# Optimization experiments

Measured on AMD Instinct MI355X. Metric: run time of the kernel, lower is better.

The kernel has to match this reference:

```python
import jax, jax.numpy as jnp
import numpy as np

N_ORDERS = 4  # edge groups processed sequentially by EmulsionConv


def setup_inputs() -> dict:
    key = jax.random.key(0)
    ks = jax.random.split(key, 12)
    N, E, D_IN, H, D_OUT, ED = 50000, 800000, 10, 64, 10, 1
    s = 0.1
    return {
        "x": jax.random.normal(ks[0], (N, D_IN), jnp.float32),
        "edge_index": jax.random.randint(ks[1], (2, E), 0, N, jnp.int32),
        "edge_features": jax.random.normal(ks[2], (E, ED), jnp.float32),
        "lin0_w": jax.random.normal(ks[3], (D_IN, H), jnp.float32) * s,
        "lin0_b": jnp.zeros((H,), jnp.float32),
        "lin1_w": jax.random.normal(ks[4], (H, H), jnp.float32) * s,
        "lin1_b": jnp.zeros((H,), jnp.float32),
        "lin2_w": jax.random.normal(ks[5], (H, H), jnp.float32) * s,
        "lin2_b": jnp.zeros((H,), jnp.float32),
        "em_w": jax.random.normal(ks[6], (3, 2 * H + ED, H), jnp.float32) * s,
        "em_b": jnp.zeros((3, H), jnp.float32),
        "ec_w": jax.random.normal(ks[7], (3, 2 * H, H), jnp.float32) * s,
        "ec_b": jnp.zeros((3, H), jnp.float32),
        "out_w": jax.random.normal(ks[8], (H, D_OUT), jnp.float32) * s,
        "out_b": jnp.zeros((D_OUT,), jnp.float32),
    }


def _emulsion_conv(x, edge_index, edge_features, w, b):
    # Sequential per-order gather -> MLP message -> scatter-add; direction=0 (aggregate at source).
    N = x.shape[0]
    E = edge_index.shape[1]
    per = E // N_ORDERS
    for i in range(N_ORDERS):
        sl = slice(i * per, (i + 1) * per)
        src = edge_index[0, sl]
        dst = edge_index[1, sl]
        x_j = x[src]  # [per, H]
        x_i = x[dst]  # [per, H]
        msg = jnp.concatenate([x_i, x_j - x_i, edge_features[sl]], axis=1)
        msg = jax.nn.relu(msg @ w + b)
        agg = jax.ops.segment_sum(msg, src, num_segments=N)
        x = (x + agg) / 2.0
    return x


def _edge_conv(x, edge_index, w, b):
    # EdgeConv: nn([x_i, x_j - x_i]) with max aggregation at target nodes.
    N = x.shape[0]
    src, dst = edge_index[0], edge_index[1]
    x_i = x[dst]
    x_j = x[src]
    msg = jax.nn.relu(jnp.concatenate([x_i, x_j - x_i], axis=1) @ w + b)
    agg = jax.ops.segment_max(msg, dst, num_segments=N)
    return jnp.where(jnp.isfinite(agg), agg, 0.0)  # empty segments -> 0


def reference(x, edge_index, edge_features,
              lin0_w, lin0_b, lin1_w, lin1_b, lin2_w, lin2_b,
              em_w, em_b, ec_w, ec_b, out_w, out_b):
    lin_ws = [lin0_w, lin1_w, lin2_w]
    lin_bs = [lin0_b, lin1_b, lin2_b]
    for i in range(3):
        x = jax.nn.relu(x @ lin_ws[i] + lin_bs[i])
        x = _emulsion_conv(x, edge_index, edge_features, em_w[i], em_b[i])
    for i in range(3):
        x = _edge_conv(x, edge_index, ec_w[i], ec_b[i])
    return x @ out_w + out_b
```

## Files before the change

### kernel.cpp

```cpp
#include <hip/hip_runtime.h>
#include <hip/hip_fp16.h>


#define NN 50000
#define NE 800000
#define PER 200000
#define HD 64
#define NKEY 250112
#define GB_CNT 3125
#define GB_PREP 192
#define GB_LIN 782
#define GB_KEYS 977

typedef _Float16 half8 __attribute__((ext_vector_type(8)));
typedef float float4v __attribute__((ext_vector_type(4)));

struct UvLds {
    _Float16 wuh[64 * 72], wul[64 * 72], wvh[64 * 72], wvl[64 * 72];
    _Float16 rp[4 * 16 * 72];
};

__global__ __launch_bounds__(256) void k_front(
        const int* __restrict__ ei, int* __restrict__ cnt,
        uchar2* __restrict__ rank,
        const float* __restrict__ em_w, const float* __restrict__ ec_w,
        _Float16* __restrict__ wh,
        const float* __restrict__ xin, const float* __restrict__ W0,
        const float* __restrict__ b0, float* __restrict__ x) {
    __shared__ float xs[64][11];
    int t = threadIdx.x;
    if (blockIdx.x < GB_CNT) {
        int e = blockIdx.x * 256 + t;
        int src = ei[e];
        int dst = ei[NE + e];
        int o = e / PER;
        int r1 = atomicAdd(&cnt[o * NN + src], 1);
        int r2 = atomicAdd(&cnt[4 * NN + dst], 1);
        rank[e] = make_uchar2((unsigned char)r1, (unsigned char)r2);
    } else if (blockIdx.x < GB_CNT + GB_PREP) {
        int idx = (blockIdx.x - GB_CNT) * 256 + t;
        int mat = idx >> 12, pos = idx & 4095;
        int n = pos >> 6, k = pos & 63;
        float val;
        if (mat < 3)      { const float* B = em_w + mat * 129 * 64;     val = B[k*64+n] - B[(64+k)*64+n]; }
        else if (mat < 6) { const float* B = em_w + (mat-3) * 129 * 64; val = B[(64+k)*64+n]; }
        else if (mat < 9) { const float* B = ec_w + (mat-6) * 128 * 64; val = B[k*64+n] - B[(64+k)*64+n]; }
        else              { const float* B = ec_w + (mat-9) * 128 * 64; val = B[(64+k)*64+n]; }
        _Float16 h = (_Float16)val;
        _Float16 l = (_Float16)(val - (float)h);
        wh[(size_t)mat * 4096 + n * 64 + k] = h;
        wh[(size_t)(12 + mat) * 4096 + n * 64 + k] = l;
    } else {
        const int K = 10;
        int n0 = (blockIdx.x - GB_CNT - GB_PREP) * 64;
        for (int idx = t; idx < 64 * K; idx += 256) {
            int n = idx / K, k = idx - n * K;
            int g = n0 + n;
            xs[n][k] = (g < NN) ? xin[(size_t)g * K + k] : 0.f;
        }
        __syncthreads();
        int ng = t >> 4;
        int f0 = (t & 15) * 4;
        float acc[4][4] = {};
        for (int k = 0; k < K; ++k) {
            float4 w4 = *(const float4*)&W0[k * HD + f0];
            #pragma unroll
            for (int j = 0; j < 4; ++j) {
                float xv = xs[ng * 4 + j][k];
                acc[j][0] += xv * w4.x; acc[j][1] += xv * w4.y;
                acc[j][2] += xv * w4.z; acc[j][3] += xv * w4.w;
            }
        }
        float4 b4 = *(const float4*)&b0[f0];
        #pragma unroll
        for (int j = 0; j < 4; ++j) {
            int g = n0 + ng * 4 + j;
            if (g < NN) {
                float4 o;
                o.x = fmaxf(acc[j][0] + b4.x, 0.f);
                o.y = fmaxf(acc[j][1] + b4.y, 0.f);
                o.z = fmaxf(acc[j][2] + b4.z, 0.f);
                o.w = fmaxf(acc[j][3] + b4.w, 0.f);
                *(float4*)&x[(size_t)g * HD + f0] = o;
            }
        }
    }
}

__global__ __launch_bounds__(256) void scan_blk(
        const int* __restrict__ cnt, int* __restrict__ bsum) {
    __shared__ int s[256];
    int t = threadIdx.x;
    int i = blockIdx.x * 256 + t;
    int c = (i < NKEY) ? cnt[i] : 0;
    s[t] = c; __syncthreads();
    for (int d = 1; d < 256; d <<= 1) {
        int v = (t >= d) ? s[t - d] : 0;
        __syncthreads(); s[t] += v; __syncthreads();
    }
    if (t == 255) bsum[blockIdx.x] = s[255];
}

__global__ __launch_bounds__(256) void scan_fin2(
        const int* __restrict__ cnt, const int* __restrict__ bsum,
        int* __restrict__ ofs) {
    __shared__ int s[256];
    int t = threadIdx.x;
    int i = blockIdx.x * 256 + t;
    int pre = 0;
    for (int j = t; j < blockIdx.x; j += 256) pre += bsum[j];
    s[t] = pre; __syncthreads();
    for (int d = 128; d > 0; d >>= 1) {
        if (t < d) s[t] += s[t + d];
        __syncthreads();
    }
    int base = s[0];
    __syncthreads();
    int c = (i < NKEY) ? cnt[i] : 0;
    s[t] = c; __syncthreads();
    for (int d = 1; d < 256; d <<= 1) {
        int v = (t >= d) ? s[t - d] : 0;
        __syncthreads(); s[t] += v; __syncthreads();
    }
    if (i < NKEY) ofs[i] = base + s[t] - c;
}

__device__ __forceinline__ void uv_body(
        UvLds& L, int bid, const float* __restrict__ x,
        const _Float16* __restrict__ Wuh, const _Float16* __restrict__ Wul,
        const _Float16* __restrict__ Wvh, const _Float16* __restrict__ Wvl,
        const float* __restrict__ bias,
        _Float16* __restrict__ u, _Float16* __restrict__ v) {
    int t = threadIdx.x;
    int n0 = bid * 64;
    {
        int n = t >> 2, c = (t & 3) * 16;
        *(half8*)&L.wuh[n * 72 + c]     = *(const half8*)&Wuh[n * 64 + c];
        *(half8*)&L.wuh[n * 72 + c + 8] = *(const half8*)&Wuh[n * 64 + c + 8];
        *(half8*)&L.wul[n * 72 + c]     = *(const half8*)&Wul[n * 64 + c];
        *(half8*)&L.wul[n * 72 + c + 8] = *(const half8*)&Wul[n * 64 + c + 8];
        *(half8*)&L.wvh[n * 72 + c]     = *(const half8*)&Wvh[n * 64 + c];
        *(half8*)&L.wvh[n * 72 + c + 8] = *(const half8*)&Wvh[n * 64 + c + 8];
        *(half8*)&L.wvl[n * 72 + c]     = *(const half8*)&Wvl[n * 64 + c];
        *(half8*)&L.wvl[n * 72 + c + 8] = *(const half8*)&Wvl[n * 64 + c + 8];
    }
    int w = t >> 6, lane = t & 63;
    int quad = lane >> 4, l16 = lane & 15;
    int m0 = w * 16;
    int row = n0 + m0 + l16;
    half8 ah0, ah1, al0, al1;
    {
        float f[16];
        if (row < NN) {
            const float4* p = (const float4*)&x[(size_t)row * HD + quad * 8];
            *(float4*)&f[0] = p[0]; *(float4*)&f[4] = p[1];
            const float4* q = (const float4*)&x[(size_t)row * HD + 32 + quad * 8];
            *(float4*)&f[8] = q[0]; *(float4*)&f[12] = q[1];
        } else {
            #pragma unroll
            for (int j = 0; j < 16; ++j) f[j] = 0.f;
        }
        #pragma unroll
        for (int j = 0; j < 8; ++j) {
            _Float16 h = (_Float16)f[j];
            ah0[j] = h; al0[j] = (_Float16)(f[j] - (float)h);
            _Float16 h2 = (_Float16)f[j + 8];
            ah1[j] = h2; al1[j] = (_Float16)(f[j + 8] - (float)h2);
        }
    }
    __syncthreads();

    float4v au[4], av[4];
    #pragma unroll
    for (int nt = 0; nt < 4; ++nt) {
        int n = nt * 16 + l16;
        half8 bh0 = *(half8*)&L.wuh[n * 72 + quad * 8];
        half8 bh1 = *(half8*)&L.wuh[n * 72 + 32 + quad * 8];
        half8 bl0 = *(half8*)&L.wul[n * 72 + quad * 8];
        half8 bl1 = *(half8*)&L.wul[n * 72 + 32 + quad * 8];
        float4v acc = {0.f, 0.f, 0.f, 0.f};
        acc = __builtin_amdgcn_mfma_f32_16x16x32_f16(ah0, bh0, acc, 0, 0, 0);
        acc = __builtin_amdgcn_mfma_f32_16x16x32_f16(ah1, bh1, acc, 0, 0, 0);
        acc = __builtin_amdgcn_mfma_f32_16x16x32_f16(al0, bh0, acc, 0, 0, 0);
        acc = __builtin_amdgcn_mfma_f32_16x16x32_f16(al1, bh1, acc, 0, 0, 0);
        acc = __builtin_amdgcn_mfma_f32_16x16x32_f16(ah0, bl0, acc, 0, 0, 0);
        acc = __builtin_amdgcn_mfma_f32_16x16x32_f16(ah1, bl1, acc, 0, 0, 0);
        au[nt] = acc;
        half8 ch0 = *(half8*)&L.wvh[n * 72 + quad * 8];
        half8 ch1 = *(half8*)&L.wvh[n * 72 + 32 + quad * 8];
        half8 cl0 = *(half8*)&L.wvl[n * 72 + quad * 8];
        half8 cl1 = *(half8*)&L.wvl[n * 72 + 32 + quad * 8];
        float4v accv = {0.f, 0.f, 0.f, 0.f};
        accv = __builtin_amdgcn_mfma_f32_16x16x32_f16(ah0, ch0, accv, 0, 0, 0);
        accv = __builtin_amdgcn_mfma_f32_16x16x32_f16(ah1, ch1, accv, 0, 0, 0);
        accv = __builtin_amdgcn_mfma_f32_16x16x32_f16(al0, ch0, accv, 0, 0, 0);
        accv = __builtin_amdgcn_mfma_f32_16x16x32_f16(al1, ch1, accv, 0, 0, 0);
        accv = __builtin_amdgcn_mfma_f32_16x16x32_f16(ah0, cl0, accv, 0, 0, 0);
        accv = __builtin_amdgcn_mfma_f32_16x16x32_f16(ah1, cl1, accv, 0, 0, 0);
        av[nt] = accv;
    }

    _Float16* rpw = &L.rp[w * 16 * 72];
    #pragma unroll
    for (int nt = 0; nt < 4; ++nt) {
        float bn = bias[nt * 16 + l16];
        #pragma unroll
        for (int r = 0; r < 4; ++r)
            rpw[(quad * 4 + r) * 72 + nt * 16 + l16] = (_Float16)(au[nt][r] + bn);
    }
    int mr = lane >> 2, cr = (lane & 3) * 16;
    int gr = n0 + m0 + mr;
    if (gr < NN) {
        *(half8*)&u[(size_t)gr * HD + cr]     = *(half8*)&rpw[mr * 72 + cr];
        *(half8*)&u[(size_t)gr * HD + cr + 8] = *(half8*)&rpw[mr * 72 + cr + 8];
    }
    #pragma unroll
    for (int nt = 0; nt < 4; ++nt) {
        #pragma unroll
        for (int r = 0; r < 4; ++r)
            rpw[(quad * 4 + r) * 72 + nt * 16 + l16] = (_Float16)(av[nt][r]);
    }
    if (gr < NN) {
        *(half8*)&v[(size_t)gr * HD + cr]     = *(half8*)&rpw[mr * 72 + cr];
        *(half8*)&v[(size_t)gr * HD + cr + 8] = *(half8*)&rpw[mr * 72 + cr + 8];
    }
}

__global__ __launch_bounds__(256) void uv_slim(
        const float* __restrict__ x,
        const _Float16* __restrict__ Wuh, const _Float16* __restrict__ Wul,
        const _Float16* __restrict__ Wvh, const _Float16* __restrict__ Wvl,
        const float* __restrict__ bias,
        _Float16* __restrict__ u, _Float16* __restrict__ v) {
    __shared__ UvLds L;
    uv_body(L, blockIdx.x, x, Wuh, Wul, Wvh, Wvl, bias, u, v);
}

__global__ __launch_bounds__(256) void k_fill_uv(
        const int* __restrict__ ei, const float* __restrict__ ef,
        const int* __restrict__ ofs, const uchar2* __restrict__ rank,
        unsigned* __restrict__ em_val, int* __restrict__ ec_val,
        const float* __restrict__ x,
        const _Float16* __restrict__ Wuh, const _Float16* __restrict__ Wul,
        const _Float16* __restrict__ Wvh, const _Float16* __restrict__ Wvl,
        const float* __restrict__ bias,
        _Float16* __restrict__ u, _Float16* __restrict__ v) {
    __shared__ UvLds L;
    if (blockIdx.x < GB_CNT) {
        int e = blockIdx.x * 256 + threadIdx.x;
        int src = ei[e];
        int dst = ei[NE + e];
        int o = e / PER;
        uchar2 r = rank[e];
        int p1 = ofs[o * NN + src] + r.x;
        unsigned short eb = __half_as_ushort(__float2half_rn(ef[e]));
        em_val[p1] = ((unsigned)dst << 16) | (unsigned)eb;
        int p2 = ofs[4 * NN + dst] + r.y - NE;
        ec_val[p2] = src;
    } else {
        uv_body(L, blockIdx.x - GB_CNT, x, Wuh, Wul, Wvh, Wvl, bias, u, v);
    }
}

__device__ __forceinline__ void load_h8(const __half* p, float* o) {
    float4 r = *(const float4*)p;
    __half2 h0 = *reinterpret_cast<__half2*>(&r.x);
    __half2 h1 = *reinterpret_cast<__half2*>(&r.y);
    __half2 h2 = *reinterpret_cast<__half2*>(&r.z);
    __half2 h3 = *reinterpret_cast<__half2*>(&r.w);
    float2 f0 = __half22float2(h0), f1 = __half22float2(h1);
    float2 f2 = __half22float2(h2), f3 = __half22float2(h3);
    o[0] = f0.x; o[1] = f0.y; o[2] = f1.x; o[3] = f1.y;
    o[4] = f2.x; o[5] = f2.y; o[6] = f3.x; o[7] = f3.y;
}

__device__ __forceinline__ void cvt_h8(float4 r, float* o) {
    __half2 h0 = *reinterpret_cast<__half2*>(&r.x);
    __half2 h1 = *reinterpret_cast<__half2*>(&r.y);
    __half2 h2 = *reinterpret_cast<__half2*>(&r.z);
    __half2 h3 = *reinterpret_cast<__half2*>(&r.w);
    float2 f0 = __half22float2(h0), f1 = __half22float2(h1);
    float2 f2 = __half22float2(h2), f3 = __half22float2(h3);
    o[0] = f0.x; o[1] = f0.y; o[2] = f1.x; o[3] = f1.y;
    o[4] = f2.x; o[5] = f2.y; o[6] = f3.x; o[7] = f3.y;
}

__device__ __forceinline__ void em_consume(
        unsigned e, float4 r, const float* vn, const float* wef, float* acc) {
    float uj[8];
    cvt_h8(r, uj);
    float ef = __half2float(__ushort_as_half((unsigned short)(e & 0xffff)));
    #pragma unroll
    for (int j = 0; j < 8; ++j)
        acc[j] += fmaxf(uj[j] + vn[j] + ef * wef[j], 0.f);
}

__global__ __launch_bounds__(256) void em_edge(
        const unsigned* __restrict__ em_val, const int* __restrict__ ofs,
        const __half* __restrict__ u, const __half* __restrict__ v,
        const float* __restrict__ we, float* __restrict__ x, int order) {
    int t = threadIdx.x;
    int node = blockIdx.x * 32 + (t >> 3);
    if (node >= NN) return;
    int f0 = (t & 7) * 8;
    int key = order * NN + node;
    int s0 = ofs[key], s1 = ofs[key + 1];
    float vn[8], wef[8], acc[8] = {};
    load_h8(&v[(size_t)node * HD + f0], vn);
    *(float4*)&wef[0] = *(const float4*)&we[f0];
    *(float4*)&wef[4] = *(const float4*)&we[f0 + 4];
    int p = s0, n = s1 - s0;
    unsigned ia0 = 0, ia1 = 0, ja0 = 0, ja1 = 0;
    float4 ra, rb;
    if (n >= 2) {
        ia0 = em_val[p]; ia1 = em_val[p + 1];
        ra = *(const float4*)&u[(size_t)(ia0 >> 16) * HD + f0];
        rb = *(const float4*)&u[(size_t)(ia1 >> 16) * HD + f0];
    }
    if (n >= 4) { ja0 = em_val[p + 2]; ja1 = em_val[p + 3]; }
    for (; p + 6 <= s1; p += 2) {
        float4 qa = *(const float4*)&u[(size_t)(ja0 >> 16) * HD + f0];
        float4 qb = *(const float4*)&u[(size_t)(ja1 >> 16) * HD + f0];
        unsigned ka0 = em_val[p + 4], ka1 = em_val[p + 5];
        em_consume(ia0, ra, vn, wef, acc);
        em_consume(ia1, rb, vn, wef, acc);
        ia0 = ja0; ia1 = ja1; ra = qa; rb = qb; ja0 = ka0; ja1 = ka1;
    }
    if (n >= 4) {
        float4 qa = *(const float4*)&u[(size_t)(ja0 >> 16) * HD + f0];
        float4 qb = *(const float4*)&u[(size_t)(ja1 >> 16) * HD + f0];
        em_consume(ia0, ra, vn, wef, acc);
        em_consume(ia1, rb, vn, wef, acc);
        em_consume(ja0, qa, vn, wef, acc);
        em_consume(ja1, qb, vn, wef, acc);
        p += 4;
    } else if (n >= 2) {
        em_consume(ia0, ra, vn, wef, acc);
        em_consume(ia1, rb, vn, wef, acc);
        p += 2;
    }
    if (p < s1) {
        unsigned e0 = em_val[p];
        float4 r0 = *(const float4*)&u[(size_t)(e0 >> 16) * HD + f0];
        em_consume(e0, r0, vn, wef, acc);
    }
    float xr[8];
    *(float4*)&xr[0] = *(const float4*)&x[(size_t)node * HD + f0];
    *(float4*)&xr[4] = *(const float4*)&x[(size_t)node * HD + f0 + 4];
    #pragma unroll
    for (int j = 0; j < 8; ++j) xr[j] = (xr[j] + acc[j]) * 0.5f;
    *(float4*)&x[(size_t)node * HD + f0] = *(float4*)&xr[0];
    *(float4*)&x[(size_t)node * HD + f0 + 4] = *(float4*)&xr[4];
}

__device__ __forceinline__ void ec_consume(float4 r, half8& m) {
    union { float4 f; half8 h; } uu; uu.f = r;
    m = __builtin_elementwise_max(m, uu.h);
}

__global__ __launch_bounds__(256) void ec_edge(
        const int* __restrict__ ec_val, const int* __restrict__ ofs,
        const __half* __restrict__ u, const __half* __restrict__ v,
        float* __restrict__ x) {
    int t = threadIdx.x;
    int node = blockIdx.x * 32 + (t >> 3);
    if (node >= NN) return;
    int f0 = (t & 7) * 8;
    int s0 = ofs[4 * NN + node] - NE, s1 = ofs[4 * NN + node + 1] - NE;
    int n = s1 - s0;
    float o[8];
    if (n > 0) {
        half8 m8;
        #pragma unroll
        for (int j = 0; j < 8; ++j) m8[j] = (_Float16)(-65504.f);
        int p = s0;
        int ja0 = 0, ja1 = 0;
        float4 ra, rb;
        if (n >= 2) {
            int ia0 = ec_val[p], ia1 = ec_val[p + 1];
            ra = *(const float4*)&v[(size_t)ia0 * HD + f0];
            rb = *(const float4*)&v[(size_t)ia1 * HD + f0];
        }
        if (n >= 4) { ja0 = ec_val[p + 2]; ja1 = ec_val[p + 3]; }
        for (; p + 6 <= s1; p += 2) {
            float4 qa = *(const float4*)&v[(size_t)ja0 * HD + f0];
            float4 qb = *(const float4*)&v[(size_t)ja1 * HD + f0];
            int ka0 = ec_val[p + 4], ka1 = ec_val[p + 5];
            ec_consume(ra, m8);
            ec_consume(rb, m8);
            ra = qa; rb = qb; ja0 = ka0; ja1 = ka1;
        }
        if (n >= 4) {
            float4 qa = *(const float4*)&v[(size_t)ja0 * HD + f0];
            float4 qb = *(const float4*)&v[(size_t)ja1 * HD + f0];
            ec_consume(ra, m8);
            ec_consume(rb, m8);
            ec_consume(qa, m8);
            ec_consume(qb, m8);
            p += 4;
        } else if (n >= 2) {
            ec_consume(ra, m8);
            ec_consume(rb, m8);
            p += 2;
        }
        if (p < s1) {
            int i0 = ec_val[p];
            float4 r0 = *(const float4*)&v[(size_t)i0 * HD + f0];
            ec_consume(r0, m8);
        }
        float un[8];
        load_h8(&u[(size_t)node * HD + f0], un);
        #pragma unroll
        for (int j = 0; j < 8; ++j)
            o[j] = fmaxf(un[j] + (float)m8[j], 0.f);
    } else {
        #pragma unroll
        for (int j = 0; j < 8; ++j) o[j] = 0.f;
    }
    *(float4*)&x[(size_t)node * HD + f0] = *(float4*)&o[0];
    *(float4*)&x[(size_t)node * HD + f0 + 4] = *(float4*)&o[4];
}

template<int K>
__global__ __launch_bounds__(256) void lin_kernel(
        const float* __restrict__ xin,
        const float* __restrict__ W, const float* __restrict__ bias,
        float* __restrict__ xout) {
    __shared__ float xs[64][K + 1];
    int t = threadIdx.x;
    int n0 = blockIdx.x * 64;
    for (int idx = t; idx < 64 * K; idx += 256) {
        int n = idx / K, k = idx - n * K;
        int g = n0 + n;
        xs[n][k] = (g < NN) ? xin[(size_t)g * K + k] : 0.f;
    }
    __syncthreads();
    int ng = t >> 4;
    int f0 = (t & 15) * 4;
    float acc[4][4] = {};
    for (int k = 0; k < K; ++k) {
        float4 w4 = *(const float4*)&W[k * HD + f0];
        #pragma unroll
        for (int j = 0; j < 4; ++j) {
            float xv = xs[ng * 4 + j][k];
            acc[j][0] += xv * w4.x; acc[j][1] += xv * w4.y;
            acc[j][2] += xv * w4.z; acc[j][3] += xv * w4.w;
        }
    }
    float4 b4 = *(const float4*)&bias[f0];
    #pragma unroll
    for (int j = 0; j < 4; ++j) {
        int g = n0 + ng * 4 + j;
        if (g < NN) {
            float4 o;
            o.x = fmaxf(acc[j][0] + b4.x, 0.f);
            o.y = fmaxf(acc[j][1] + b4.y, 0.f);
            o.z = fmaxf(acc[j][2] + b4.z, 0.f);
            o.w = fmaxf(acc[j][3] + b4.w, 0.f);
            *(float4*)&xout[(size_t)g * HD + f0] = o;
        }
    }
}

__global__ __launch_bounds__(256) void out_kernel(
        const float* __restrict__ x, const float* __restrict__ W,
        const float* __restrict__ bias, float* __restrict__ out) {
    int n = blockIdx.x * 256 + threadIdx.x;
    if (n >= NN) return;
    float acc[10];
    #pragma unroll
    for (int f = 0; f < 10; ++f) acc[f] = bias[f];
    #pragma unroll
    for (int k0 = 0; k0 < HD; k0 += 16) {
        float xr[16];
        #pragma unroll
        for (int k = 0; k < 16; k += 4)
            *(float4*)&xr[k] = *(const float4*)&x[(size_t)n * HD + k0 + k];
        #pragma unroll
        for (int k = 0; k < 16; ++k) {
            #pragma unroll
            for (int f = 0; f < 10; ++f)
                acc[f] += xr[k] * W[(k0 + k) * 10 + f];
        }
    }
    #pragma unroll
    for (int f = 0; f < 10; ++f) out[(size_t)n * 10 + f] = acc[f];
}

extern "C" void kernel_launch(void* const* d_in, const int* in_sizes, int n_in,
                              void* d_out, int out_size, void* d_ws, size_t ws_size,
                              hipStream_t stream) {
    const float* x_in  = (const float*)d_in[0];
    const int*   ei    = (const int*)d_in[1];
    const float* ef    = (const float*)d_in[2];
    const float* lw[3] = {(const float*)d_in[3], (const float*)d_in[5], (const float*)d_in[7]};
    const float* lb[3] = {(const float*)d_in[4], (const float*)d_in[6], (const float*)d_in[8]};
    const float* em_w  = (const float*)d_in[9];
    const float* em_b  = (const float*)d_in[10];
    const float* ec_w  = (const float*)d_in[11];
    const float* ec_b  = (const float*)d_in[12];
    const float* ow    = (const float*)d_in[13];
    const float* ob    = (const float*)d_in[14];
    float* out = (float*)d_out;

    char* wsb = (char*)d_ws;
    size_t off = 0;
    auto alloc = [&](size_t bytes) {
        void* p = wsb + off;
        off = (off + bytes + 255) & ~(size_t)255;
        return p;
    };
    float*     x      = (float*)alloc((size_t)NN * HD * 4);
    _Float16*  u      = (_Float16*)alloc((size_t)NN * HD * 2);
    _Float16*  v      = (_Float16*)alloc((size_t)NN * HD * 2);
    int*       cnt    = (int*)alloc((size_t)NKEY * 4);
    int*       ofs    = (int*)alloc((size_t)NKEY * 4);
    int*       bsum   = (int*)alloc((size_t)1024 * 4);
    uchar2*    rank   = (uchar2*)alloc((size_t)NE * 2);
    unsigned*  em_val = (unsigned*)alloc((size_t)NE * 4);
    int*       ec_val = (int*)alloc((size_t)NE * 4);
    _Float16*  wh     = (_Float16*)alloc((size_t)24 * 4096 * 2);
    (void)ws_size; (void)in_sizes; (void)n_in; (void)out_size;

    const int gb_n8 = (NN + 31) / 32;

    hipMemsetAsync(cnt, 0, (size_t)NKEY * 4, stream);
    k_front<<<GB_CNT + GB_PREP + GB_LIN, 256, 0, stream>>>(
        ei, cnt, rank, em_w, ec_w, wh, x_in, lw[0], lb[0], x);
    scan_blk<<<GB_KEYS, 256, 0, stream>>>(cnt, bsum);
    scan_fin2<<<GB_KEYS, 256, 0, stream>>>(cnt, bsum, ofs);

    k_fill_uv<<<GB_CNT + GB_LIN, 256, 0, stream>>>(
        ei, ef, ofs, rank, em_val, ec_val, x,
        wh, wh + (size_t)12 * 4096, wh + (size_t)3 * 4096, wh + (size_t)15 * 4096,
        em_b, u, v);

    for (int i = 0; i < 3; ++i) {
        const _Float16* Wuh = wh + (size_t)i * 4096;
        const _Float16* Wvh = wh + (size_t)(3 + i) * 4096;
        const _Float16* Wul = wh + (size_t)(12 + i) * 4096;
        const _Float16* Wvl = wh + (size_t)(15 + i) * 4096;
        const float* bi = em_b + (size_t)i * HD;
        const float* we = em_w + (size_t)i * 129 * HD + 128 * HD;
        for (int o = 0; o < 4; ++o) {
            if (!(i == 0 && o == 0))
                uv_slim<<<GB_LIN, 256, 0, stream>>>(x, Wuh, Wul, Wvh, Wvl, bi, u, v);
            em_edge<<<gb_n8, 256, 0, stream>>>(em_val, ofs, (const __half*)u,
                                               (const __half*)v, we, x, o);
        }
        if (i < 2)
            lin_kernel<64><<<GB_LIN, 256, 0, stream>>>(x, lw[i + 1], lb[i + 1], x);
    }

    for (int j = 0; j < 3; ++j) {
        const _Float16* Wuh = wh + (size_t)(6 + j) * 4096;
        const _Float16* Wvh = wh + (size_t)(9 + j) * 4096;
        const _Float16* Wul = wh + (size_t)(18 + j) * 4096;
        const _Float16* Wvl = wh + (size_t)(21 + j) * 4096;
        const float* bj = ec_b + (size_t)j * HD;
        uv_slim<<<GB_LIN, 256, 0, stream>>>(x, Wuh, Wul, Wvh, Wvl, bj, u, v);
        ec_edge<<<gb_n8, 256, 0, stream>>>(ec_val, ofs, (const __half*)u,
                                           (const __half*)v, x);
    }

    out_kernel<<<(NN + 255) / 256, 256, 0, stream>>>(x, ow, ob, out);
}
```

Measured before the change: 572.9 us.

## Fuse emulsion edge aggregation with next-order u/v projection kernel

Adds an emuv kernel that aggregates one edge order per node, updates x, and then immediately computes the next order's u/v projections with MFMA from the updated x tile held in LDS. Ping-pong u/v buffers are used because other blocks may still gather from the previous u. This removes a separate uv_slim launch and its reread of x for three of the four orders per layer. The cost is lower parallelism in the edge phase, since each thread now handles 16 features, plus more LDS per block.

```diff
diff --git a/kernel.cpp b/kernel.cpp
--- a/kernel.cpp
+++ b/kernel.cpp
@@ -18,6 +18,14 @@
 struct UvLds {
     _Float16 wuh[64 * 72], wul[64 * 72], wvh[64 * 72], wvl[64 * 72];
     _Float16 rp[4 * 16 * 72];
+};
+
+struct EmuvLds {
+    union {
+        float xs[64][68];
+        _Float16 rp[4 * 16 * 72];
+    } a;
+    _Float16 wuh[64 * 72], wvh[64 * 72];
 };
 
 __global__ __launch_bounds__(256) void k_front(
@@ -285,6 +293,162 @@
     o[4] = f2.x; o[5] = f2.y; o[6] = f3.x; o[7] = f3.y;
 }
 
+__global__ __launch_bounds__(256) void emuv(
+        const unsigned* __restrict__ em_val, const int* __restrict__ ofs,
+        const __half* __restrict__ u_in, const __half* __restrict__ v_in,
+        const float* __restrict__ we, int order, float* __restrict__ x,
+        const _Float16* __restrict__ Wuh, const _Float16* __restrict__ Wul,
+        const _Float16* __restrict__ Wvh, const _Float16* __restrict__ Wvl,
+        const float* __restrict__ bias,
+        _Float16* __restrict__ u_out, _Float16* __restrict__ v_out) {
+    __shared__ EmuvLds L;
+    int t = threadIdx.x;
+    int n0 = blockIdx.x * 64;
+    {
+        int n = t >> 2, c = (t & 3) * 16;
+        *(half8*)&L.wuh[n * 72 + c]     = *(const half8*)&Wuh[n * 64 + c];
+        *(half8*)&L.wuh[n * 72 + c + 8] = *(const half8*)&Wuh[n * 64 + c + 8];
+        *(half8*)&L.wvh[n * 72 + c]     = *(const half8*)&Wvh[n * 64 + c];
+        *(half8*)&L.wvh[n * 72 + c + 8] = *(const half8*)&Wvh[n * 64 + c + 8];
+    }
+    {
+        int nd = t >> 2, sub = t & 3, f0 = sub * 16;
+        int node = n0 + nd;
+        if (node < NN) {
+            float vn[16], wef[16], acc[16] = {};
+            load_h8(&v_in[(size_t)node * HD + f0], vn);
+            load_h8(&v_in[(size_t)node * HD + f0 + 8], vn + 8);
+            *(float4*)&wef[0]  = *(const float4*)&we[f0];
+            *(float4*)&wef[4]  = *(const float4*)&we[f0 + 4];
+            *(float4*)&wef[8]  = *(const float4*)&we[f0 + 8];
+            *(float4*)&wef[12] = *(const float4*)&we[f0 + 12];
+            int key = order * NN + node;
+            int s0 = ofs[key], s1 = ofs[key + 1];
+            int p = s0;
+            for (; p + 2 <= s1; p += 2) {
+                unsigned e0 = em_val[p], e1 = em_val[p + 1];
+                const __half* r0 = &u_in[(size_t)(e0 >> 16) * HD + f0];
+                const __half* r1 = &u_in[(size_t)(e1 >> 16) * HD + f0];
+                float u0[16], u1[16];
+                load_h8(r0, u0); load_h8(r0 + 8, u0 + 8);
+                load_h8(r1, u1); load_h8(r1 + 8, u1 + 8);
+                float ef0 = __half2float(__ushort_as_half((unsigned short)(e0 & 0xffff)));
+                float ef1 = __half2float(__ushort_as_half((unsigned short)(e1 & 0xffff)));
+                #pragma unroll
+                for (int j = 0; j < 16; ++j) {
+                    acc[j] += fmaxf(u0[j] + vn[j] + ef0 * wef[j], 0.f)
+                            + fmaxf(u1[j] + vn[j] + ef1 * wef[j], 0.f);
+                }
+            }
+            if (p < s1) {
+                unsigned e0 = em_val[p];
+                const __half* r0 = &u_in[(size_t)(e0 >> 16) * HD + f0];
+                float u0[16];
+                load_h8(r0, u0); load_h8(r0 + 8, u0 + 8);
+                float ef0 = __half2float(__ushort_as_half((unsigned short)(e0 & 0xffff)));
+                #pragma unroll
+                for (int j = 0; j < 16; ++j)
+                    acc[j] += fmaxf(u0[j] + vn[j] + ef0 * wef[j], 0.f);
+            }
+            float xr[16];
+            *(float4*)&xr[0]  = *(const float4*)&x[(size_t)node * HD + f0];
+            *(float4*)&xr[4]  = *(const float4*)&x[(size_t)node * HD + f0 + 4];
+            *(float4*)&xr[8]  = *(const float4*)&x[(size_t)node * HD + f0 + 8];
+            *(float4*)&xr[12] = *(const float4*)&x[(size_t)node * HD + f0 + 12];
+            #pragma unroll
+            for (int j = 0; j < 16; ++j) xr[j] = (xr[j] + acc[j]) * 0.5f;
+            *(float4*)&x[(size_t)node * HD + f0]      = *(float4*)&xr[0];
+            *(float4*)&x[(size_t)node * HD + f0 + 4]  = *(float4*)&xr[4];
+            *(float4*)&x[(size_t)node * HD + f0 + 8]  = *(float4*)&xr[8];
+            *(float4*)&x[(size_t)node * HD + f0 + 12] = *(float4*)&xr[12];
+            *(float4*)&L.a.xs[nd][f0]      = *(float4*)&xr[0];
+            *(float4*)&L.a.xs[nd][f0 + 4]  = *(float4*)&xr[4];
+            *(float4*)&L.a.xs[nd][f0 + 8]  = *(float4*)&xr[8];
+            *(float4*)&L.a.xs[nd][f0 + 12] = *(float4*)&xr[12];
+        } else {
+            float4 z = {0.f, 0.f, 0.f, 0.f};
+            *(float4*)&L.a.xs[nd][f0]      = z;
+            *(float4*)&L.a.xs[nd][f0 + 4]  = z;
+            *(float4*)&L.a.xs[nd][f0 + 8]  = z;
+            *(float4*)&L.a.xs[nd][f0 + 12] = z;
+        }
+    }
+    __syncthreads();
+    int w = t >> 6, lane = t & 63;
+    int quad = lane >> 4, l16 = lane & 15;
+    int m0 = w * 16;
+    int rowl = m0 + l16;
+    half8 ah0, ah1, al0, al1;
+    {
+        float f[16];
+        *(float4*)&f[0]  = *(float4*)&L.a.xs[rowl][quad * 8];
+        *(float4*)&f[4]  = *(float4*)&L.a.xs[rowl][quad * 8 + 4];
+        *(float4*)&f[8]  = *(float4*)&L.a.xs[rowl][32 + quad * 8];
+        *(float4*)&f[12] = *(float4*)&L.a.xs[rowl][32 + quad * 8 + 4];
+        #pragma unroll
+        for (int j = 0; j < 8; ++j) {
+            _Float16 h = (_Float16)f[j];
+            ah0[j] = h; al0[j] = (_Float16)(f[j] - (float)h);
+            _Float16 h2 = (_Float16)f[j + 8];
+            ah1[j] = h2; al1[j] = (_Float16)(f[j + 8] - (float)h2);
+        }
+    }
+    float4v au[4], av[4];
+    #pragma unroll
+    for (int nt = 0; nt < 4; ++nt) {
+        int n = nt * 16 + l16;
+        half8 bh0 = *(half8*)&L.wuh[n * 72 + quad * 8];
+        half8 bh1 = *(half8*)&L.wuh[n * 72 + 32 + quad * 8];
+        half8 bl0 = *(const half8*)&Wul[n * 64 + quad * 8];
+        half8 bl1 = *(const half8*)&Wul[n * 64 + 32 + quad * 8];
+        float4v acc = {0.f, 0.f, 0.f, 0.f};
+        acc = __builtin_amdgcn_mfma_f32_16x16x32_f16(ah0, bh0, acc, 0, 0, 0);
+        acc = __builtin_amdgcn_mfma_f32_16x16x32_f16(ah1, bh1, acc, 0, 0, 0);
+        acc = __builtin_amdgcn_mfma_f32_16x16x32_f16(al0, bh0, acc, 0, 0, 0);
+        acc = __builtin_amdgcn_mfma_f32_16x16x32_f16(al1, bh1, acc, 0, 0, 0);
+        acc = __builtin_amdgcn_mfma_f32_16x16x32_f16(ah0, bl0, acc, 0, 0, 0);
+        acc = __builtin_amdgcn_mfma_f32_16x16x32_f16(ah1, bl1, acc, 0, 0, 0);
+        au[nt] = acc;
+        half8 ch0 = *(half8*)&L.wvh[n * 72 + quad * 8];
+        half8 ch1 = *(half8*)&L.wvh[n * 72 + 32 + quad * 8];
+        half8 cl0 = *(const half8*)&Wvl[n * 64 + quad * 8];
+        half8 cl1 = *(const half8*)&Wvl[n * 64 + 32 + quad * 8];
+        float4v accv = {0.f, 0.f, 0.f, 0.f};
+        accv = __builtin_amdgcn_mfma_f32_16x16x32_f16(ah0, ch0, accv, 0, 0, 0);
+        accv = __builtin_amdgcn_mfma_f32_16x16x32_f16(ah1, ch1, accv, 0, 0, 0);
+        accv = __builtin_amdgcn_mfma_f32_16x16x32_f16(al0, ch0, accv, 0, 0, 0);
+        accv = __builtin_amdgcn_mfma_f32_16x16x32_f16(al1, ch1, accv, 0, 0, 0);
+        accv = __builtin_amdgcn_mfma_f32_16x16x32_f16(ah0, cl0, accv, 0, 0, 0);
+        accv = __builtin_amdgcn_mfma_f32_16x16x32_f16(ah1, cl1, accv, 0, 0, 0);
+        av[nt] = accv;
+    }
+    __syncthreads();
+    _Float16* rpw = &L.a.rp[w * 16 * 72];
+    #pragma unroll
+    for (int nt = 0; nt < 4; ++nt) {
+        float bn = bias[nt * 16 + l16];
+        #pragma unroll
+        for (int r = 0; r < 4; ++r)
+            rpw[(quad * 4 + r) * 72 + nt * 16 + l16] = (_Float16)(au[nt][r] + bn);
+    }
+    int mr = lane >> 2, cr = (lane & 3) * 16;
+    int gr = n0 + m0 + mr;
+    if (gr < NN) {
+        *(half8*)&u_out[(size_t)gr * HD + cr]     = *(half8*)&rpw[mr * 72 + cr];
+        *(half8*)&u_out[(size_t)gr * HD + cr + 8] = *(half8*)&rpw[mr * 72 + cr + 8];
+    }
+    #pragma unroll
+    for (int nt = 0; nt < 4; ++nt) {
+        #pragma unroll
+        for (int r = 0; r < 4; ++r)
+            rpw[(quad * 4 + r) * 72 + nt * 16 + l16] = (_Float16)(av[nt][r]);
+    }
+    if (gr < NN) {
+        *(half8*)&v_out[(size_t)gr * HD + cr]     = *(half8*)&rpw[mr * 72 + cr];
+        *(half8*)&v_out[(size_t)gr * HD + cr + 8] = *(half8*)&rpw[mr * 72 + cr + 8];
+    }
+}
+
 __device__ __forceinline__ void em_consume(
         unsigned e, float4 r, const float* vn, const float* wef, float* acc) {
     float uj[8];
@@ -513,6 +677,8 @@
     float*     x      = (float*)alloc((size_t)NN * HD * 4);
     _Float16*  u      = (_Float16*)alloc((size_t)NN * HD * 2);
     _Float16*  v      = (_Float16*)alloc((size_t)NN * HD * 2);
+    _Float16*  u2     = (_Float16*)alloc((size_t)NN * HD * 2);
+    _Float16*  v2     = (_Float16*)alloc((size_t)NN * HD * 2);
     int*       cnt    = (int*)alloc((size_t)NKEY * 4);
     int*       ofs    = (int*)alloc((size_t)NKEY * 4);
     int*       bsum   = (int*)alloc((size_t)1024 * 4);
@@ -542,12 +708,16 @@
         const _Float16* Wvl = wh + (size_t)(15 + i) * 4096;
         const float* bi = em_b + (size_t)i * HD;
         const float* we = em_w + (size_t)i * 129 * HD + 128 * HD;
-        for (int o = 0; o < 4; ++o) {
-            if (!(i == 0 && o == 0))
-                uv_slim<<<GB_LIN, 256, 0, stream>>>(x, Wuh, Wul, Wvh, Wvl, bi, u, v);
-            em_edge<<<gb_n8, 256, 0, stream>>>(em_val, ofs, (const __half*)u,
-                                               (const __half*)v, we, x, o);
-        }
+        if (i > 0)
+            uv_slim<<<GB_LIN, 256, 0, stream>>>(x, Wuh, Wul, Wvh, Wvl, bi, u, v);
+        emuv<<<GB_LIN, 256, 0, stream>>>(em_val, ofs, (const __half*)u,
+            (const __half*)v, we, 0, x, Wuh, Wul, Wvh, Wvl, bi, u2, v2);
+        emuv<<<GB_LIN, 256, 0, stream>>>(em_val, ofs, (const __half*)u2,
+            (const __half*)v2, we, 1, x, Wuh, Wul, Wvh, Wvl, bi, u, v);
+        emuv<<<GB_LIN, 256, 0, stream>>>(em_val, ofs, (const __half*)u,
+            (const __half*)v, we, 2, x, Wuh, Wul, Wvh, Wvl, bi, u2, v2);
+        em_edge<<<gb_n8, 256, 0, stream>>>(em_val, ofs, (const __half*)u2,
+                                           (const __half*)v2, we, x, 3);
         if (i < 2)
             lin_kernel<64><<<GB_LIN, 256, 0, stream>>>(x, lw[i + 1], lb[i + 1], x);
     }
```

Result: slower. 607.6 us (+6.1%).
